# Performance work log

Hardware: AMD Instinct MI355X
Metric: run time of the kernel (lower is better)

The kernel has to match this reference:

```python
import jax, jax.numpy as jnp
import numpy as np

B, SQ, FDIM = 32, 196, 2048
L, EDIM, H = 1000, 1024, 16
DH = EDIM // H  # 64


def setup_inputs() -> dict:
    key = jax.random.key(0)
    ks = jax.random.split(key, 10)
    s = lambda fan_in: 1.0 / np.sqrt(fan_in)
    return {
        "features": jax.random.normal(ks[0], (B, SQ, FDIM), jnp.float32),
        "label_embeddings": jax.random.normal(ks[1], (L, EDIM), jnp.float32),
        "Wq": jax.random.normal(ks[2], (EDIM, FDIM), jnp.float32) * s(FDIM),
        "bq": jax.random.normal(ks[3], (EDIM,), jnp.float32) * s(FDIM),
        "Wk": jax.random.normal(ks[4], (EDIM, EDIM), jnp.float32) * s(EDIM),
        "bk": jax.random.normal(ks[5], (EDIM,), jnp.float32) * s(EDIM),
        "Wv": jax.random.normal(ks[6], (EDIM, EDIM), jnp.float32) * s(EDIM),
        "bv": jax.random.normal(ks[7], (EDIM,), jnp.float32) * s(EDIM),
        "Wo": jax.random.normal(ks[8], (EDIM, EDIM), jnp.float32) * s(EDIM),
        "bo": jax.random.normal(ks[9], (EDIM,), jnp.float32) * s(EDIM),
    }


def reference(features, label_embeddings, Wq, bq, Wk, bk, Wv, bv, Wo, bo):
    # Q projection: [B, Sq, E] -> [B, Sq, H, Dh]
    q = (jnp.einsum("bsf,ef->bse", features, Wq) + bq).reshape(B, SQ, H, DH)
    # K/V projections on the shared label table: [L, E] -> [L, H, Dh]
    k = (label_embeddings @ Wk.T + bk).reshape(L, H, DH)
    v = (label_embeddings @ Wv.T + bv).reshape(L, H, DH)
    # scores: [B, H, Sq, L]
    scores = jnp.einsum("bqhd,lhd->bhql", q, k) / jnp.sqrt(jnp.float32(DH))
    attn = jax.nn.softmax(scores, axis=-1)
    # attention output: [B, Sq, H, Dh] -> [B, Sq, E]
    ctx = jnp.einsum("bhql,lhd->bqhd", attn, v).reshape(B, SQ, EDIM)
    return jnp.einsum("bse,oe->bso", ctx, Wo) + bo
```

## Files before the change

kernel.cpp:

```cpp
#include <hip/hip_runtime.h>
#include <hip/hip_bf16.h>
#include <stdint.h>
#include <math.h>

constexpr int BB   = 32;
constexpr int SQ   = 196;
constexpr int FDIM = 2048;
constexpr int LL   = 1000;
constexpr int EDIM = 1024;
constexpr int HH   = 16;
constexpr int BSQ  = BB * SQ;

typedef unsigned short u16;
typedef unsigned int   u32;
typedef __attribute__((ext_vector_type(4)))  float f32x4;
typedef __attribute__((ext_vector_type(16))) float f32x16;
typedef __attribute__((ext_vector_type(8)))  short bf16x8;
typedef __attribute__((ext_vector_type(2)))  int   i32x2;

#define DEV __device__ __forceinline__

DEV u16 f2bf(float f) {
  unsigned u = __float_as_uint(f);
  unsigned r = 0x7FFFu + ((u >> 16) & 1u);
  return (u16)((u + r) >> 16);
}

DEV u32 pack2bf(float a, float b) {
  __hip_bfloat162 h = __float22bfloat162_rn(float2{a, b});
  return *reinterpret_cast<const u32*>(&h);
}

#if __has_builtin(__builtin_amdgcn_exp2f)
#define EXP2F(x) __builtin_amdgcn_exp2f(x)
#else
#define EXP2F(x) exp2f(x)
#endif

DEV f32x16 zero16() {
  f32x16 v;
#pragma unroll
  for (int i = 0; i < 16; ++i) v[i] = 0.f;
  return v;
}

#if __has_builtin(__builtin_amdgcn_permlane32_swap)
DEV void half_swap(u32& a, u32& b, int ) {
  i32x2 r = __builtin_amdgcn_permlane32_swap((int)a, (int)b, false, false);
  a = (u32)r[0]; b = (u32)r[1];
}
#else
DEV void half_swap(u32& a, u32& b, int hi) {
  const u32 sa = __shfl_xor(a, 32), sb = __shfl_xor(b, 32);
  const u32 na = hi ? sb : a;
  const u32 nb = hi ? b : sa;
  a = na; b = nb;
}
#endif

#define GLDS16(g, l) __builtin_amdgcn_global_load_lds(                         \
    (const __attribute__((address_space(1))) void*)(g),                       \
    (__attribute__((address_space(3))) void*)(l), 16, 0, 0)

DEV int xcd_chunk(int bid, int cpx) { return (bid & 7) * cpx + (bid >> 3); }

constexpr int C_N0 = EDIM * FDIM / 4;
constexpr int C_N1 = C_N0 + EDIM * EDIM / 4;
constexpr int C_N2 = C_N1 + EDIM * EDIM / 4;
constexpr int C_N3 = C_N2 + EDIM * EDIM / 4;
constexpr int C_N4 = C_N3 + LL * EDIM / 4;

__global__ void cvt_all(const float* __restrict__ wq,
                        const float* __restrict__ wk, const float* __restrict__ wv,
                        const float* __restrict__ wo, const float* __restrict__ lab,
                        u16* dwq, u16* dwk, u16* dwv, u16* dwo, u16* dlab) {
  int i = blockIdx.x * blockDim.x + threadIdx.x;
  const int st = gridDim.x * blockDim.x;
  for (; i < C_N4; i += st) {
    const float* s; u16* d; int j;
    if (i < C_N0)      { s = wq;  d = dwq;  j = i; }
    else if (i < C_N1) { s = wk;  d = dwk;  j = i - C_N0; }
    else if (i < C_N2) { s = wv;  d = dwv;  j = i - C_N1; }
    else if (i < C_N3) { s = wo;  d = dwo;  j = i - C_N2; }
    else               { s = lab; d = dlab; j = i - C_N3; }
    float4 v = reinterpret_cast<const float4*>(s)[j];
    ushort4 o;
    o.x = f2bf(v.x); o.y = f2bf(v.y); o.z = f2bf(v.z); o.w = f2bf(v.w);
    reinterpret_cast<ushort4*>(d)[j] = o;
  }
}

template<bool OUT_BF16, bool A_F32>
DEV void gemm_body(u16* sA, u16* sB, int bid,
                   const void* Ap_,
                   const u16* B1, const float* bias1, void* C1,
                   const u16* B2, const float* bias2, void* C2,
                   int M, int K, int ntn, int ntiles_n1, float scale, int c2t) {
  const int tn  = bid % ntn;
  const int tm  = bid / ntn;

  const u16* Bp; const float* biasp; void* Cp; int tnl; bool tw;
  if (tn < ntiles_n1) { Bp = B1; biasp = bias1; Cp = C1; tnl = tn; tw = false; }
  else { Bp = B2; biasp = bias2; Cp = C2; tnl = tn - ntiles_n1; tw = (c2t != 0); }

  const int lane = threadIdx.x & 63;
  const int wid  = threadIdx.x >> 6;
  const int wr   = wid >> 1, wc = wid & 1;
  const int lr   = lane & 15, lg = lane >> 4;

  f32x4 acc[4][4];
#pragma unroll
  for (int m = 0; m < 4; ++m)
#pragma unroll
    for (int n = 0; n < 4; ++n) acc[m][n] = (f32x4){0.f, 0.f, 0.f, 0.f};

  for (int k0 = 0; k0 < K; k0 += 64) {
    if (A_F32) {
      const float* A32 = (const float*)Ap_;
#pragma unroll
      for (int i = 0; i < 4; ++i) {
        const int chunk = wid * 4 + i;
        const int row   = chunk * 8 + (lane >> 3);
        const size_t off = (size_t)(tm * 128 + row) * K + k0 + (lane & 7) * 8;
        const float4 f0 = *reinterpret_cast<const float4*>(A32 + off);
        const float4 f1 = *reinterpret_cast<const float4*>(A32 + off + 4);
        uint4 w;
        w.x = pack2bf(f0.x, f0.y); w.y = pack2bf(f0.z, f0.w);
        w.z = pack2bf(f1.x, f1.y); w.w = pack2bf(f1.z, f1.w);
        *reinterpret_cast<uint4*>(&sA[chunk * 512 + lane * 8]) = w;
      }
    } else {
      const u16* Abf = (const u16*)Ap_;
#pragma unroll
      for (int i = 0; i < 4; ++i) {
        const int chunk = wid * 4 + i;
        const int row   = chunk * 8 + (lane >> 3);
        int ga = tm * 128 + row; ga = ga < M ? ga : M - 1;
        GLDS16(Abf + (size_t)ga * K + k0 + (lane & 7) * 8, &sA[chunk * 512]);
      }
    }
#pragma unroll
    for (int i = 0; i < 4; ++i) {
      const int chunk = wid * 4 + i;
      const int row   = chunk * 8 + (lane >> 3);
      const int gb = tnl * 128 + row;
      GLDS16(Bp + (size_t)gb * K + k0 + (lane & 7) * 8, &sB[chunk * 512]);
    }
    asm volatile("s_waitcnt vmcnt(0)" ::: "memory");
    __syncthreads();
#pragma unroll
    for (int ks = 0; ks < 2; ++ks) {
      bf16x8 af[4], bfr[4];
#pragma unroll
      for (int m = 0; m < 4; ++m)
        af[m] = *reinterpret_cast<const bf16x8*>(&sA[(wr * 64 + m * 16 + lr) * 64 + ks * 32 + lg * 8]);
#pragma unroll
      for (int n = 0; n < 4; ++n)
        bfr[n] = *reinterpret_cast<const bf16x8*>(&sB[(wc * 64 + n * 16 + lr) * 64 + ks * 32 + lg * 8]);
#pragma unroll
      for (int m = 0; m < 4; ++m)
#pragma unroll
        for (int n = 0; n < 4; ++n)
          acc[m][n] = __builtin_amdgcn_mfma_f32_16x16x32_bf16(af[m], bfr[n], acc[m][n], 0, 0, 0);
    }
    __syncthreads();
  }

#pragma unroll
  for (int n = 0; n < 4; ++n) {
    const int c  = tnl * 128 + wc * 64 + n * 16 + lr;
    const float bv = biasp[c];
#pragma unroll
    for (int m = 0; m < 4; ++m) {
#pragma unroll
      for (int r = 0; r < 4; ++r) {
        const int rr = tm * 128 + wr * 64 + m * 16 + lg * 4 + r;
        const float v = (acc[m][n][r] + bv) * scale;
        if (OUT_BF16) {
          if (tw)
            ((u16*)Cp)[(size_t)c * 1024 + rr] = (rr < M) ? f2bf(v) : (u16)0;
          else if (rr < M)
            ((u16*)Cp)[(size_t)rr * 1024 + c] = f2bf(v);
        } else if (rr < M)
          ((float*)Cp)[(size_t)rr * 1024 + c] = v;
      }
    }
  }
}

__global__ __launch_bounds__(256)
void gemm_proj_fused(const float* fA, const u16* wq, const float* bq, u16* qo,
                     const u16* lA, const u16* wk, const float* bk, u16* ko,
                     const u16* wv, const float* bv, u16* vto,
                     float qscale) {
  __shared__ __attribute__((aligned(16))) u16 sA[128 * 64];
  __shared__ __attribute__((aligned(16))) u16 sB[128 * 64];
  const int bid = blockIdx.x;
  if (bid < 392) {
    const int nb = xcd_chunk(bid, 49);
    gemm_body<true, true>(sA, sB, nb, fA, wq, bq, qo,
                          nullptr, nullptr, nullptr, BSQ, FDIM, 8, 8, qscale, 0);
  } else {
    int nb = xcd_chunk(bid - 392, 16);
    nb = (nb % 8) * 16 + (nb / 8);
    gemm_body<true, false>(sA, sB, nb, lA, wk, bk, ko,
                           wv, bv, vto, LL, EDIM, 16, 8, 1.0f, 1);
  }
}

__global__ __launch_bounds__(256)
void gemm_oproj(const u16* __restrict__ A, const u16* __restrict__ B,
                const float* __restrict__ bias, float* __restrict__ C) {
  __shared__ __attribute__((aligned(16))) u16 sA[64 * 64];
  __shared__ __attribute__((aligned(16))) u16 sB[128 * 64];
  const int nb = xcd_chunk(blockIdx.x, 98);
  const int tn = nb % 8, tm = nb / 8;

  const int lane = threadIdx.x & 63;
  const int wid  = threadIdx.x >> 6;
  const int lr = lane & 15, lg = lane >> 4;

  f32x4 acc[4][2];
#pragma unroll
  for (int m = 0; m < 4; ++m)
#pragma unroll
    for (int n = 0; n < 2; ++n) acc[m][n] = (f32x4){0.f, 0.f, 0.f, 0.f};

  for (int k0 = 0; k0 < EDIM; k0 += 64) {
#pragma unroll
    for (int i = 0; i < 2; ++i) {
      const int chunk = wid * 2 + i;
      const int row = chunk * 8 + (lane >> 3);
      GLDS16(A + (size_t)(tm * 64 + row) * 1024 + k0 + (lane & 7) * 8, &sA[chunk * 512]);
    }
#pragma unroll
    for (int i = 0; i < 4; ++i) {
      const int chunk = wid * 4 + i;
      const int row = chunk * 8 + (lane >> 3);
      GLDS16(B + (size_t)(tn * 128 + row) * 1024 + k0 + (lane & 7) * 8, &sB[chunk * 512]);
    }
    asm volatile("s_waitcnt vmcnt(0)" ::: "memory");
    __syncthreads();
#pragma unroll
    for (int ks = 0; ks < 2; ++ks) {
      bf16x8 af[4], bfr[2];
#pragma unroll
      for (int m = 0; m < 4; ++m)
        af[m] = *reinterpret_cast<const bf16x8*>(&sA[(m * 16 + lr) * 64 + ks * 32 + lg * 8]);
#pragma unroll
      for (int n = 0; n < 2; ++n)
        bfr[n] = *reinterpret_cast<const bf16x8*>(&sB[(wid * 32 + n * 16 + lr) * 64 + ks * 32 + lg * 8]);
#pragma unroll
      for (int m = 0; m < 4; ++m)
#pragma unroll
        for (int n = 0; n < 2; ++n)
          acc[m][n] = __builtin_amdgcn_mfma_f32_16x16x32_bf16(af[m], bfr[n], acc[m][n], 0, 0, 0);
    }
    __syncthreads();
  }

#pragma unroll
  for (int n = 0; n < 2; ++n) {
    const int c = tn * 128 + wid * 32 + n * 16 + lr;
    const float bv = bias[c];
#pragma unroll
    for (int m = 0; m < 4; ++m) {
#pragma unroll
      for (int r = 0; r < 4; ++r) {
        const int rr = tm * 64 + m * 16 + lg * 4 + r;
        C[(size_t)rr * 1024 + c] = acc[m][n][r] + bv;
      }
    }
  }
}

__global__ __launch_bounds__(256, 2)
void attn_kernel(const u16* __restrict__ Q, const u16* __restrict__ Kb,
                 const u16* __restrict__ VT, u16* __restrict__ ctx) {
  const int wg = xcd_chunk(blockIdx.x, 98);
  const int h = wg / 49, qb = wg % 49;
  __shared__ __attribute__((aligned(16))) u16 sm[16384];

  const int t    = threadIdx.x;
  const int lane = t & 63;
  const int wid  = t >> 6;
  const int l31  = lane & 31, hi = lane >> 5;

  const int qrow = qb * 128 + wid * 32 + l31;
  const u16* qp = Q + (size_t)qrow * EDIM + h * 64;
  bf16x8 qf[4];
#pragma unroll
  for (int ks = 0; ks < 4; ++ks)
    qf[ks] = *reinterpret_cast<const bf16x8*>(qp + ks * 16 + hi * 8);

  f32x16 ctxa[2]; ctxa[0] = zero16(); ctxa[1] = zero16();
  float lsum = 0.f;

  auto stage = [&](int buf, int l0s) {
#pragma unroll
    for (int i = 0; i < 2; ++i) {
      const int chunk = wid * 2 + i;
      const int row   = chunk * 8 + (lane >> 3);
      const int sl    = (lane & 7) ^ (row & 7);
      int lk = l0s + row; if (lk > LL - 1) lk = LL - 1;
      GLDS16(Kb + (size_t)lk * EDIM + h * 64 + sl * 8, sm + buf * 4096 + chunk * 512);
      GLDS16(VT + (size_t)(h * 64 + row) * 1024 + l0s + sl * 8, sm + 8192 + buf * 4096 + chunk * 512);
    }
  };
  auto frag = [&](const u16* base, int row, int slot) -> bf16x8 {
    return *reinterpret_cast<const bf16x8*>(base + row * 64 + ((slot ^ (row & 7)) * 8));
  };

  constexpr int NT = (LL + 63) / 64;
  stage(0, 0);
  asm volatile("s_waitcnt vmcnt(0)" ::: "memory");
  __syncthreads();

  for (int it = 0; it < NT; ++it) {
    const int l0  = it * 64;
    const int cur = it & 1;
    if (it + 1 < NT) stage(cur ^ 1, l0 + 64);

    const u16* sKb = sm + cur * 4096;
    const u16* sVb = sm + 8192 + cur * 4096;

    f32x16 st[2]; st[0] = zero16(); st[1] = zero16();
    __builtin_amdgcn_s_setprio(1);
#pragma unroll
    for (int ks = 0; ks < 4; ++ks) {
#pragma unroll
      for (int jt = 0; jt < 2; ++jt) {
        bf16x8 kf = frag(sKb, jt * 32 + l31, 2 * ks + hi);
        st[jt] = __builtin_amdgcn_mfma_f32_32x32x16_bf16(kf, qf[ks], st[jt], 0, 0, 0);
      }
    }
    __builtin_amdgcn_s_setprio(0);

    u32 pk[2][4][2];
    auto softmax_pack = [&](bool tail) {
#pragma unroll
      for (int jt = 0; jt < 2; ++jt) {
#pragma unroll
        for (int g = 0; g < 4; ++g) {
          float p[4];
#pragma unroll
          for (int j = 0; j < 4; ++j) {
            float e = EXP2F(st[jt][g * 4 + j]);
            if (tail) {
              const int kg = l0 + jt * 32 + j + 8 * g + 4 * hi;
              if (kg >= LL) e = 0.f;
            }
            p[j] = e;
            lsum += e;
          }
          pk[jt][g][0] = pack2bf(p[0], p[1]);
          pk[jt][g][1] = pack2bf(p[2], p[3]);
        }
      }
    };
    if (l0 + 64 <= LL) softmax_pack(false); else softmax_pack(true);

    __builtin_amdgcn_s_setprio(1);
#pragma unroll
    for (int ksl = 0; ksl < 4; ++ksl) {
      const int jt = ksl >> 1, e2 = ksl & 1;
      u32 x0 = pk[jt][2 * e2 + 0][0], y0 = pk[jt][2 * e2 + 1][0];
      u32 x1 = pk[jt][2 * e2 + 0][1], y1 = pk[jt][2 * e2 + 1][1];
      half_swap(x0, y0, hi);
      half_swap(x1, y1, hi);
      union { u32 d[4]; bf16x8 v; } pf;
      pf.d[0] = x0; pf.d[1] = x1; pf.d[2] = y0; pf.d[3] = y1;
#pragma unroll
      for (int dt = 0; dt < 2; ++dt) {
        bf16x8 vf = frag(sVb, dt * 32 + l31, 2 * ksl + hi);
        ctxa[dt] = __builtin_amdgcn_mfma_f32_32x32x16_bf16(vf, pf.v, ctxa[dt], 0, 0, 0);
      }
    }
    __builtin_amdgcn_s_setprio(0);

    asm volatile("s_waitcnt vmcnt(0)" ::: "memory");
    __syncthreads();
  }

  float ltot = lsum + __shfl_xor(lsum, 32);
  const float inv = 1.0f / ltot;

  u16* tb = sm;
  const int q = wid * 32 + l31;
#pragma unroll
  for (int dt = 0; dt < 2; ++dt) {
#pragma unroll
    for (int g = 0; g < 4; ++g) {
      u32 w0 = pack2bf(ctxa[dt][g * 4 + 0] * inv, ctxa[dt][g * 4 + 1] * inv);
      u32 w1 = pack2bf(ctxa[dt][g * 4 + 2] * inv, ctxa[dt][g * 4 + 3] * inv);
      const int d2   = dt * 64 + g * 16 + hi * 8;
      const int byte = q * 128 + (d2 ^ ((q & 7) << 4));
      *reinterpret_cast<u32*>(reinterpret_cast<char*>(tb) + byte)     = w0;
      *reinterpret_cast<u32*>(reinterpret_cast<char*>(tb) + byte + 4) = w1;
    }
  }
  __syncthreads();
#pragma unroll
  for (int pass = 0; pass < 4; ++pass) {
    const int row  = pass * 32 + (t >> 3);
    const int srow = qb * 128 + row;
    const int cb = ((t & 7) * 16) ^ ((row & 7) << 4);
    uint4 val = *reinterpret_cast<const uint4*>(reinterpret_cast<const char*>(tb) + row * 128 + cb);
    *reinterpret_cast<uint4*>(ctx + (size_t)srow * EDIM + h * 64 + (t & 7) * 8) = val;
  }
}

extern "C" void kernel_launch(void* const* d_in, const int* in_sizes, int n_in,
                              void* d_out, int out_size, void* d_ws, size_t ws_size,
                              hipStream_t stream) {
  const float* features = (const float*)d_in[0];
  const float* labels   = (const float*)d_in[1];
  const float* Wq = (const float*)d_in[2];
  const float* bq = (const float*)d_in[3];
  const float* Wk = (const float*)d_in[4];
  const float* bk = (const float*)d_in[5];
  const float* Wv = (const float*)d_in[6];
  const float* bv = (const float*)d_in[7];
  const float* Wo = (const float*)d_in[8];
  const float* bo = (const float*)d_in[9];
  float* out = (float*)d_out;

  u16* wq_bf  = (u16*)d_ws;
  u16* wk_bf  = wq_bf  + (size_t)EDIM * FDIM;
  u16* wv_bf  = wk_bf  + (size_t)EDIM * EDIM;
  u16* wo_bf  = wv_bf  + (size_t)EDIM * EDIM;
  u16* lab_bf = wo_bf  + (size_t)EDIM * EDIM;
  u16* q_bf   = lab_bf + (size_t)LL   * EDIM;
  u16* k_bf   = q_bf   + (size_t)BSQ  * EDIM;
  u16* vt_bf  = k_bf   + (size_t)LL   * EDIM;
  u16* ctx_bf = vt_bf  + (size_t)1024 * 1024;

  cvt_all<<<1024, 256, 0, stream>>>(Wq, Wk, Wv, Wo, labels,
                                    wq_bf, wk_bf, wv_bf, wo_bf, lab_bf);

  const float qscale = 0.125f * 1.4426950408889634f;
  gemm_proj_fused<<<49 * 8 + 8 * 16, 256, 0, stream>>>(
      features, wq_bf, bq, q_bf, lab_bf, wk_bf, bk, k_bf, wv_bf, bv, vt_bf, qscale);

  attn_kernel<<<784, 256, 0, stream>>>(q_bf, k_bf, vt_bf, ctx_bf);

  gemm_oproj<<<784, 256, 0, stream>>>(ctx_bf, wo_bf, bo, out);
}
```

Before: 154.8 us.

## Move K/V projection into prep kernel and pre-convert features for Q GEMM

The K/V projection now runs inside the conversion kernel, reading fp32 labels and weights directly and converting on the fly, while the other blocks convert features, Wq and Wo to bf16. The Q projection becomes its own 64x128-tile GEMM using async global-to-LDS loads on the pre-converted bf16 features instead of converting fp32 in registers. This trades an extra full read and write pass over the features for a simpler, async-loaded Q GEMM with more blocks. It also removes the separate conversion of Wk, Wv and the labels.

```diff
diff --git a/kernel.cpp b/kernel.cpp
--- a/kernel.cpp
+++ b/kernel.cpp
@@ -64,44 +64,15 @@
 
 DEV int xcd_chunk(int bid, int cpx) { return (bid & 7) * cpx + (bid >> 3); }
 
-constexpr int C_N0 = EDIM * FDIM / 4;
-constexpr int C_N1 = C_N0 + EDIM * EDIM / 4;
-constexpr int C_N2 = C_N1 + EDIM * EDIM / 4;
-constexpr int C_N3 = C_N2 + EDIM * EDIM / 4;
-constexpr int C_N4 = C_N3 + LL * EDIM / 4;
-
-__global__ void cvt_all(const float* __restrict__ wq,
-                        const float* __restrict__ wk, const float* __restrict__ wv,
-                        const float* __restrict__ wo, const float* __restrict__ lab,
-                        u16* dwq, u16* dwk, u16* dwv, u16* dwo, u16* dlab) {
-  int i = blockIdx.x * blockDim.x + threadIdx.x;
-  const int st = gridDim.x * blockDim.x;
-  for (; i < C_N4; i += st) {
-    const float* s; u16* d; int j;
-    if (i < C_N0)      { s = wq;  d = dwq;  j = i; }
-    else if (i < C_N1) { s = wk;  d = dwk;  j = i - C_N0; }
-    else if (i < C_N2) { s = wv;  d = dwv;  j = i - C_N1; }
-    else if (i < C_N3) { s = wo;  d = dwo;  j = i - C_N2; }
-    else               { s = lab; d = dlab; j = i - C_N3; }
-    float4 v = reinterpret_cast<const float4*>(s)[j];
-    ushort4 o;
-    o.x = f2bf(v.x); o.y = f2bf(v.y); o.z = f2bf(v.z); o.w = f2bf(v.w);
-    reinterpret_cast<ushort4*>(d)[j] = o;
-  }
-}
-
-template<bool OUT_BF16, bool A_F32>
-DEV void gemm_body(u16* sA, u16* sB, int bid,
-                   const void* Ap_,
-                   const u16* B1, const float* bias1, void* C1,
-                   const u16* B2, const float* bias2, void* C2,
-                   int M, int K, int ntn, int ntiles_n1, float scale, int c2t) {
-  const int tn  = bid % ntn;
-  const int tm  = bid / ntn;
-
-  const u16* Bp; const float* biasp; void* Cp; int tnl; bool tw;
-  if (tn < ntiles_n1) { Bp = B1; biasp = bias1; Cp = C1; tnl = tn; tw = false; }
-  else { Bp = B2; biasp = bias2; Cp = C2; tnl = tn - ntiles_n1; tw = (c2t != 0); }
+DEV void kv_body(u16* sA, u16* sB, int nb,
+                 const float* __restrict__ lab,
+                 const float* B1, const float* bias1, u16* C1,
+                 const float* B2, const float* bias2, u16* C2) {
+  const int tn = nb % 16;
+  const int tm = nb / 16;
+  const float* Bp; const float* biasp; u16* Cp; int tnl; bool tw;
+  if (tn < 8) { Bp = B1; biasp = bias1; Cp = C1; tnl = tn; tw = false; }
+  else        { Bp = B2; biasp = bias2; Cp = C2; tnl = tn - 8; tw = true; }
 
   const int lane = threadIdx.x & 63;
   const int wid  = threadIdx.x >> 6;
@@ -114,39 +85,27 @@
 #pragma unroll
     for (int n = 0; n < 4; ++n) acc[m][n] = (f32x4){0.f, 0.f, 0.f, 0.f};
 
-  for (int k0 = 0; k0 < K; k0 += 64) {
-    if (A_F32) {
-      const float* A32 = (const float*)Ap_;
-#pragma unroll
-      for (int i = 0; i < 4; ++i) {
-        const int chunk = wid * 4 + i;
-        const int row   = chunk * 8 + (lane >> 3);
-        const size_t off = (size_t)(tm * 128 + row) * K + k0 + (lane & 7) * 8;
-        const float4 f0 = *reinterpret_cast<const float4*>(A32 + off);
-        const float4 f1 = *reinterpret_cast<const float4*>(A32 + off + 4);
-        uint4 w;
-        w.x = pack2bf(f0.x, f0.y); w.y = pack2bf(f0.z, f0.w);
-        w.z = pack2bf(f1.x, f1.y); w.w = pack2bf(f1.z, f1.w);
-        *reinterpret_cast<uint4*>(&sA[chunk * 512 + lane * 8]) = w;
-      }
-    } else {
-      const u16* Abf = (const u16*)Ap_;
-#pragma unroll
-      for (int i = 0; i < 4; ++i) {
-        const int chunk = wid * 4 + i;
-        const int row   = chunk * 8 + (lane >> 3);
-        int ga = tm * 128 + row; ga = ga < M ? ga : M - 1;
-        GLDS16(Abf + (size_t)ga * K + k0 + (lane & 7) * 8, &sA[chunk * 512]);
-      }
-    }
+  for (int k0 = 0; k0 < EDIM; k0 += 64) {
 #pragma unroll
     for (int i = 0; i < 4; ++i) {
       const int chunk = wid * 4 + i;
       const int row   = chunk * 8 + (lane >> 3);
-      const int gb = tnl * 128 + row;
-      GLDS16(Bp + (size_t)gb * K + k0 + (lane & 7) * 8, &sB[chunk * 512]);
-    }
-    asm volatile("s_waitcnt vmcnt(0)" ::: "memory");
+      int ga = tm * 128 + row; ga = ga < LL ? ga : LL - 1;
+      const size_t ao = (size_t)ga * EDIM + k0 + (lane & 7) * 8;
+      const float4 a0 = *reinterpret_cast<const float4*>(lab + ao);
+      const float4 a1 = *reinterpret_cast<const float4*>(lab + ao + 4);
+      uint4 wa;
+      wa.x = pack2bf(a0.x, a0.y); wa.y = pack2bf(a0.z, a0.w);
+      wa.z = pack2bf(a1.x, a1.y); wa.w = pack2bf(a1.z, a1.w);
+      *reinterpret_cast<uint4*>(&sA[chunk * 512 + lane * 8]) = wa;
+      const size_t bo = (size_t)(tnl * 128 + row) * EDIM + k0 + (lane & 7) * 8;
+      const float4 b0 = *reinterpret_cast<const float4*>(Bp + bo);
+      const float4 b1 = *reinterpret_cast<const float4*>(Bp + bo + 4);
+      uint4 wb;
+      wb.x = pack2bf(b0.x, b0.y); wb.y = pack2bf(b0.z, b0.w);
+      wb.z = pack2bf(b1.x, b1.y); wb.w = pack2bf(b1.z, b1.w);
+      *reinterpret_cast<uint4*>(&sB[chunk * 512 + lane * 8]) = wb;
+    }
     __syncthreads();
 #pragma unroll
     for (int ks = 0; ks < 2; ++ks) {
@@ -175,42 +134,55 @@
 #pragma unroll
       for (int r = 0; r < 4; ++r) {
         const int rr = tm * 128 + wr * 64 + m * 16 + lg * 4 + r;
-        const float v = (acc[m][n][r] + bv) * scale;
-        if (OUT_BF16) {
-          if (tw)
-            ((u16*)Cp)[(size_t)c * 1024 + rr] = (rr < M) ? f2bf(v) : (u16)0;
-          else if (rr < M)
-            ((u16*)Cp)[(size_t)rr * 1024 + c] = f2bf(v);
-        } else if (rr < M)
-          ((float*)Cp)[(size_t)rr * 1024 + c] = v;
+        const float v = acc[m][n][r] + bv;
+        if (tw)
+          Cp[(size_t)c * 1024 + rr] = (rr < LL) ? f2bf(v) : (u16)0;
+        else if (rr < LL)
+          Cp[(size_t)rr * 1024 + c] = f2bf(v);
       }
     }
   }
 }
 
+constexpr int P_N0 = BSQ * FDIM / 4;
+constexpr int P_N1 = P_N0 + EDIM * FDIM / 4;
+constexpr int P_N2 = P_N1 + EDIM * EDIM / 4;
+constexpr int PREP_GRID = 1024;
+
 __global__ __launch_bounds__(256)
-void gemm_proj_fused(const float* fA, const u16* wq, const float* bq, u16* qo,
-                     const u16* lA, const u16* wk, const float* bk, u16* ko,
-                     const u16* wv, const float* bv, u16* vto,
-                     float qscale) {
+void prep_kernel(const float* __restrict__ lab,
+                 const float* __restrict__ wk, const float* __restrict__ bk, u16* ko,
+                 const float* __restrict__ wv, const float* __restrict__ bv, u16* vto,
+                 const float* __restrict__ f, const float* __restrict__ wq,
+                 const float* __restrict__ wo,
+                 u16* df, u16* dwq, u16* dwo) {
   __shared__ __attribute__((aligned(16))) u16 sA[128 * 64];
   __shared__ __attribute__((aligned(16))) u16 sB[128 * 64];
   const int bid = blockIdx.x;
-  if (bid < 392) {
-    const int nb = xcd_chunk(bid, 49);
-    gemm_body<true, true>(sA, sB, nb, fA, wq, bq, qo,
-                          nullptr, nullptr, nullptr, BSQ, FDIM, 8, 8, qscale, 0);
+  if (bid < 128) {
+    int nb = xcd_chunk(bid, 16);
+    nb = (nb % 8) * 16 + (nb / 8);
+    kv_body(sA, sB, nb, lab, wk, bk, ko, wv, bv, vto);
   } else {
-    int nb = xcd_chunk(bid - 392, 16);
-    nb = (nb % 8) * 16 + (nb / 8);
-    gemm_body<true, false>(sA, sB, nb, lA, wk, bk, ko,
-                           wv, bv, vto, LL, EDIM, 16, 8, 1.0f, 1);
-  }
-}
-
-__global__ __launch_bounds__(256)
-void gemm_oproj(const u16* __restrict__ A, const u16* __restrict__ B,
-                const float* __restrict__ bias, float* __restrict__ C) {
+    int i = (bid - 128) * 256 + threadIdx.x;
+    const int st = (PREP_GRID - 128) * 256;
+    for (; i < P_N2; i += st) {
+      const float* s; u16* d; int j;
+      if (i < P_N0)      { s = f;  d = df;  j = i; }
+      else if (i < P_N1) { s = wq; d = dwq; j = i - P_N0; }
+      else               { s = wo; d = dwo; j = i - P_N1; }
+      float4 v = reinterpret_cast<const float4*>(s)[j];
+      ushort4 o;
+      o.x = f2bf(v.x); o.y = f2bf(v.y); o.z = f2bf(v.z); o.w = f2bf(v.w);
+      reinterpret_cast<ushort4*>(d)[j] = o;
+    }
+  }
+}
+
+template<bool OUT_BF16>
+DEV void body64(const u16* __restrict__ A, const u16* __restrict__ B,
+                const float* __restrict__ bias, void* __restrict__ C,
+                int K, float scale) {
   __shared__ __attribute__((aligned(16))) u16 sA[64 * 64];
   __shared__ __attribute__((aligned(16))) u16 sB[128 * 64];
   const int nb = xcd_chunk(blockIdx.x, 98);
@@ -226,18 +198,18 @@
 #pragma unroll
     for (int n = 0; n < 2; ++n) acc[m][n] = (f32x4){0.f, 0.f, 0.f, 0.f};
 
-  for (int k0 = 0; k0 < EDIM; k0 += 64) {
+  for (int k0 = 0; k0 < K; k0 += 64) {
 #pragma unroll
     for (int i = 0; i < 2; ++i) {
       const int chunk = wid * 2 + i;
       const int row = chunk * 8 + (lane >> 3);
-      GLDS16(A + (size_t)(tm * 64 + row) * 1024 + k0 + (lane & 7) * 8, &sA[chunk * 512]);
+      GLDS16(A + (size_t)(tm * 64 + row) * K + k0 + (lane & 7) * 8, &sA[chunk * 512]);
     }
 #pragma unroll
     for (int i = 0; i < 4; ++i) {
       const int chunk = wid * 4 + i;
       const int row = chunk * 8 + (lane >> 3);
-      GLDS16(B + (size_t)(tn * 128 + row) * 1024 + k0 + (lane & 7) * 8, &sB[chunk * 512]);
+      GLDS16(B + (size_t)(tn * 128 + row) * K + k0 + (lane & 7) * 8, &sB[chunk * 512]);
     }
     asm volatile("s_waitcnt vmcnt(0)" ::: "memory");
     __syncthreads();
@@ -268,10 +240,22 @@
 #pragma unroll
       for (int r = 0; r < 4; ++r) {
         const int rr = tm * 64 + m * 16 + lg * 4 + r;
-        C[(size_t)rr * 1024 + c] = acc[m][n][r] + bv;
+        const float v = (acc[m][n][r] + bv) * scale;
+        if (OUT_BF16) ((u16*)C)[(size_t)rr * 1024 + c] = f2bf(v);
+        else          ((float*)C)[(size_t)rr * 1024 + c] = v;
       }
     }
   }
+}
+
+__global__ __launch_bounds__(256)
+void gemm_qproj(const u16* A, const u16* B, const float* bias, u16* C, float qscale) {
+  body64<true>(A, B, bias, C, FDIM, qscale);
+}
+
+__global__ __launch_bounds__(256)
+void gemm_oproj(const u16* A, const u16* B, const float* bias, float* C) {
+  body64<false>(A, B, bias, C, EDIM, 1.0f);
 }
 
 __global__ __launch_bounds__(256, 2)
@@ -425,22 +409,20 @@
   const float* bo = (const float*)d_in[9];
   float* out = (float*)d_out;
 
-  u16* wq_bf  = (u16*)d_ws;
-  u16* wk_bf  = wq_bf  + (size_t)EDIM * FDIM;
-  u16* wv_bf  = wk_bf  + (size_t)EDIM * EDIM;
-  u16* wo_bf  = wv_bf  + (size_t)EDIM * EDIM;
-  u16* lab_bf = wo_bf  + (size_t)EDIM * EDIM;
-  u16* q_bf   = lab_bf + (size_t)LL   * EDIM;
+  u16* f_bf   = (u16*)d_ws;
+  u16* wq_bf  = f_bf   + (size_t)BSQ  * FDIM;
+  u16* wo_bf  = wq_bf  + (size_t)EDIM * FDIM;
+  u16* q_bf   = wo_bf  + (size_t)EDIM * EDIM;
   u16* k_bf   = q_bf   + (size_t)BSQ  * EDIM;
   u16* vt_bf  = k_bf   + (size_t)LL   * EDIM;
   u16* ctx_bf = vt_bf  + (size_t)1024 * 1024;
 
-  cvt_all<<<1024, 256, 0, stream>>>(Wq, Wk, Wv, Wo, labels,
-                                    wq_bf, wk_bf, wv_bf, wo_bf, lab_bf);
+  prep_kernel<<<PREP_GRID, 256, 0, stream>>>(
+      labels, Wk, bk, k_bf, Wv, bv, vt_bf,
+      features, Wq, Wo, f_bf, wq_bf, wo_bf);
 
   const float qscale = 0.125f * 1.4426950408889634f;
-  gemm_proj_fused<<<49 * 8 + 8 * 16, 256, 0, stream>>>(
-      features, wq_bf, bq, q_bf, lab_bf, wk_bf, bk, k_bf, wv_bf, bv, vt_bf, qscale);
+  gemm_qproj<<<784, 256, 0, stream>>>(f_bf, wq_bf, bq, q_bf, qscale);
 
   attn_kernel<<<784, 256, 0, stream>>>(q_bf, k_bf, vt_bf, ctx_bf);
 
```

Result: slower. 171.6 us (+10.9%).
